# Optimization experiments

Measured on AMD Instinct MI355X. Metric: run time of the kernel, lower is better.

Reference implementation:

```python
import jax, jax.numpy as jnp
import numpy as np

MODEL_DIM = 256
PAIR_IMPORTANCE_WEIGHT = 0.5
B, S, D = 4, 4096, MODEL_DIM


def setup_inputs() -> dict:
    key = jax.random.key(0)
    ks = jax.random.split(key, 6)
    return {
        "query": jax.random.normal(ks[0], (B, S, D), dtype=jnp.float32),
        "key": jax.random.normal(ks[1], (B, S, D), dtype=jnp.float32),
        "value": jax.random.normal(ks[2], (B, S, D), dtype=jnp.float32),
        "W_query": jax.random.normal(ks[3], (D, D), dtype=jnp.float32),
        "W_key": jax.random.normal(ks[4], (D, D), dtype=jnp.float32),
        "W_value": jax.random.normal(ks[5], (D, D), dtype=jnp.float32),
    }


def reference(query, key, value, W_query, W_key, W_value):
    # Projections: [B,S,D] @ [D,D]
    q = jnp.einsum('bsd,de->bse', query, W_query)
    k = jnp.einsum('bsd,de->bse', key, W_key)
    v = jnp.einsum('bsd,de->bse', value, W_value)
    scale = jnp.sqrt(jnp.asarray(MODEL_DIM, dtype=q.dtype))
    # Full [B,S,S] score matrix (global max forces materialization)
    scores = jnp.einsum('bqd,bkd->bqk', q, k) / scale
    s_len = scores.shape[1]
    diag_bias = jnp.eye(s_len, dtype=scores.dtype) * jnp.max(scores)
    scores = scores + PAIR_IMPORTANCE_WEIGHT * diag_bias  # broadcast over batch
    attention_weights = jax.nn.softmax(scores, axis=-1)
    output = jnp.einsum('bqk,bkd->bqd', attention_weights, v)
    return output, attention_weights
```

## Files before the change

### kernel.cpp

```cpp
#include <hip/hip_runtime.h>
#include <cstdint>
#include <cstddef>

#define BB 4
#define SS 4096
#define DD 256
#define SCORE_SCALE (1.0f/16.0f)
#define PIW 0.5f

typedef float          f32x4  __attribute__((ext_vector_type(4)));
typedef __bf16         bf16v8 __attribute__((ext_vector_type(8)));
typedef unsigned short u16v8  __attribute__((ext_vector_type(8)));
typedef unsigned short u16v4  __attribute__((ext_vector_type(4)));

__device__ __forceinline__ f32x4 mfma_bf16(u16v8 a, u16v8 b, f32x4 c) {
    return __builtin_amdgcn_mfma_f32_16x16x32_bf16(
        __builtin_bit_cast(bf16v8, a), __builtin_bit_cast(bf16v8, b), c, 0, 0, 0);
}

__device__ __forceinline__ unsigned short f2bf(float f) {
    unsigned u = __float_as_uint(f);
    u += 0x7FFFu + ((u >> 16) & 1u);
    return (unsigned short)(u >> 16);
}
__device__ __forceinline__ float bf2f(unsigned short h) {
    return __uint_as_float(((unsigned)h) << 16);
}
__device__ __forceinline__ unsigned fenc(float x) {
    unsigned u = __float_as_uint(x);
    return (u & 0x80000000u) ? ~u : (u | 0x80000000u);
}
__device__ __forceinline__ float fdec(unsigned e) {
    return __uint_as_float((e & 0x80000000u) ? (e ^ 0x80000000u) : ~e);
}

#define TM 128
#define TN 128
#define TK 16
#define PADW 132

__global__ __launch_bounds__(256) void proj_kernel(
    const float* __restrict__ query, const float* __restrict__ key_, const float* __restrict__ value,
    const float* __restrict__ Wq, const float* __restrict__ Wk, const float* __restrict__ Wv,
    unsigned short* __restrict__ qh, unsigned short* __restrict__ ql,
    unsigned short* __restrict__ kh, unsigned short* __restrict__ kl,
    unsigned short* __restrict__ vT, unsigned* __restrict__ gmax)
{
    const int z = blockIdx.z;
    const float* A = (z == 0) ? query : (z == 1) ? key_ : value;
    const float* W = (z == 0) ? Wq    : (z == 1) ? Wk   : Wv;
    if (z == 0 && blockIdx.x == 0 && blockIdx.y == 0 && threadIdx.x == 0)
        *gmax = 0x007FFFFFu;

    const int K = DD, N = DD;
    __shared__ float As[TK][PADW];
    __shared__ float Bs[TK][PADW];
    const int tid = threadIdx.x;
    const int tx = tid & 15, ty = tid >> 4;
    const int rowBase = blockIdx.y * TM;
    const int colBase = blockIdx.x * TN;

    float acc[8][8] = {};

    for (int k0 = 0; k0 < K; k0 += TK) {
        #pragma unroll
        for (int i = 0; i < 2; i++) {
            int idx = tid + i * 256;
            int r = idx >> 2, kq = idx & 3;
            const float4 av = *(const float4*)&A[(size_t)(rowBase + r) * K + k0 + kq * 4];
            As[kq * 4 + 0][r] = av.x; As[kq * 4 + 1][r] = av.y;
            As[kq * 4 + 2][r] = av.z; As[kq * 4 + 3][r] = av.w;
        }
        #pragma unroll
        for (int i = 0; i < 2; i++) {
            int idx = tid + i * 256;
            int kk = idx >> 5, cq = idx & 31;
            *(float4*)&Bs[kk][cq * 4] = *(const float4*)&W[(size_t)(k0 + kk) * N + colBase + cq * 4];
        }
        __syncthreads();
        #pragma unroll
        for (int kk = 0; kk < TK; kk++) {
            float a[8], b[8];
            *(float4*)&a[0] = *(const float4*)&As[kk][ty * 8];
            *(float4*)&a[4] = *(const float4*)&As[kk][ty * 8 + 4];
            *(float4*)&b[0] = *(const float4*)&Bs[kk][tx * 8];
            *(float4*)&b[4] = *(const float4*)&Bs[kk][tx * 8 + 4];
            #pragma unroll
            for (int i = 0; i < 8; i++)
                #pragma unroll
                for (int j = 0; j < 8; j++)
                    acc[i][j] = fmaf(a[i], b[j], acc[i][j]);
        }
        __syncthreads();
    }

    #pragma unroll
    for (int i = 0; i < 8; i++) {
        const int gr = rowBase + ty * 8 + i;
        if (z == 2) {
            const int b2 = gr >> 12, s2 = gr & (SS - 1);
            #pragma unroll
            for (int j = 0; j < 8; j++) {
                int col = colBase + tx * 8 + j;
                vT[((size_t)b2 * DD + col) * SS + s2] = f2bf(acc[i][j]);
            }
        } else {
            unsigned short h[8], l[8];
            #pragma unroll
            for (int j = 0; j < 8; j++) {
                h[j] = f2bf(acc[i][j]);
                l[j] = f2bf(acc[i][j] - bf2f(h[j]));
            }
            unsigned short* H = (z == 0) ? qh : kh;
            unsigned short* L = (z == 0) ? ql : kl;
            size_t base = (size_t)gr * DD + colBase + tx * 8;
            *(u16v4*)&H[base]     = (u16v4){h[0], h[1], h[2], h[3]};
            *(u16v4*)&H[base + 4] = (u16v4){h[4], h[5], h[6], h[7]};
            *(u16v4*)&L[base]     = (u16v4){l[0], l[1], l[2], l[3]};
            *(u16v4*)&L[base + 4] = (u16v4){l[4], l[5], l[6], l[7]};
        }
    }
}

#define SPAD 40

__global__ __launch_bounds__(256) void scores_mfma(
    const unsigned short* __restrict__ qh, const unsigned short* __restrict__ ql,
    const unsigned short* __restrict__ kh, const unsigned short* __restrict__ kl,
    float* __restrict__ attn, unsigned* __restrict__ gmax)
{
    const int b = blockIdx.z;
    const size_t boff = (size_t)b * SS * DD;
    const unsigned short* Qh = qh + boff;
    const unsigned short* Ql = ql + boff;
    const unsigned short* Kh = kh + boff;
    const unsigned short* Kl = kl + boff;
    float* C = attn + (size_t)b * SS * SS;

    __shared__ unsigned short Ah[128][SPAD];
    __shared__ unsigned short Al[128][SPAD];
    __shared__ unsigned short Bh[128][SPAD];
    __shared__ unsigned short Bl[128][SPAD];
    __shared__ float red[256];

    const int tid = threadIdx.x;
    const int lane = tid & 63, w = tid >> 6;
    const int wr = (w >> 1) * 64, wc = (w & 1) * 64;
    const int m = lane & 15, qq = lane >> 4;
    const int rowBase = blockIdx.y * 128;
    const int colBase = blockIdx.x * 128;

    f32x4 acc[4][4];
    #pragma unroll
    for (int i = 0; i < 4; i++)
        #pragma unroll
        for (int j = 0; j < 4; j++)
            acc[i][j] = (f32x4){0.f, 0.f, 0.f, 0.f};

    const int chunk = (tid & 3) * 8;
    const int srow  = tid >> 2;

    for (int k0 = 0; k0 < DD; k0 += 32) {
        #pragma unroll
        for (int i = 0; i < 2; i++) {
            int r = srow + i * 64;
            size_t ga = (size_t)(rowBase + r) * DD + k0 + chunk;
            size_t gb = (size_t)(colBase + r) * DD + k0 + chunk;
            *(u16v8*)&Ah[r][chunk] = *(const u16v8*)&Qh[ga];
            *(u16v8*)&Al[r][chunk] = *(const u16v8*)&Ql[ga];
            *(u16v8*)&Bh[r][chunk] = *(const u16v8*)&Kh[gb];
            *(u16v8*)&Bl[r][chunk] = *(const u16v8*)&Kl[gb];
        }
        __syncthreads();

        const int kb = qq * 8;
        u16v8 ah[4], al[4], bh[4], bl[4];
        #pragma unroll
        for (int i = 0; i < 4; i++) {
            ah[i] = *(const u16v8*)&Ah[wr + i * 16 + m][kb];
            al[i] = *(const u16v8*)&Al[wr + i * 16 + m][kb];
            bh[i] = *(const u16v8*)&Bh[wc + i * 16 + m][kb];
            bl[i] = *(const u16v8*)&Bl[wc + i * 16 + m][kb];
        }
        #pragma unroll
        for (int i = 0; i < 4; i++)
            #pragma unroll
            for (int j = 0; j < 4; j++) {
                acc[i][j] = mfma_bf16(ah[i], bh[j], acc[i][j]);
                acc[i][j] = mfma_bf16(ah[i], bl[j], acc[i][j]);
                acc[i][j] = mfma_bf16(al[i], bh[j], acc[i][j]);
            }
        __syncthreads();
    }

    float mx = -INFINITY;
    #pragma unroll
    for (int i = 0; i < 4; i++) {
        #pragma unroll
        for (int j = 0; j < 4; j++) {
            #pragma unroll
            for (int r = 0; r < 4; r++) {
                float v = acc[i][j][r] * SCORE_SCALE;
                int row = rowBase + wr + i * 16 + qq * 4 + r;
                int col = colBase + wc + j * 16 + m;
                C[(size_t)row * SS + col] = v;
                mx = fmaxf(mx, v);
            }
        }
    }
    red[tid] = mx;
    __syncthreads();
    for (int s2 = 128; s2 > 0; s2 >>= 1) {
        if (tid < s2) red[tid] = fmaxf(red[tid], red[tid + s2]);
        __syncthreads();
    }
    if (tid == 0) atomicMax(gmax, fenc(red[0]));
}

__global__ __launch_bounds__(256) void softmax_kernel(
    float* __restrict__ attn, const unsigned* __restrict__ gmax)
{
    const int row = blockIdx.x;
    const int i = row & (SS - 1);
    float* p = attn + (size_t)row * SS;
    const float bias = PIW * fdec(*gmax);
    const int tid = threadIdx.x;

    float x[16];
    float m = -INFINITY;
    #pragma unroll
    for (int u = 0; u < 4; u++) {
        int j4 = u * 1024 + tid * 4;
        float4 t = *(const float4*)&p[j4];
        float e0 = t.x + ((j4 + 0 == i) ? bias : 0.0f);
        float e1 = t.y + ((j4 + 1 == i) ? bias : 0.0f);
        float e2 = t.z + ((j4 + 2 == i) ? bias : 0.0f);
        float e3 = t.w + ((j4 + 3 == i) ? bias : 0.0f);
        x[u * 4 + 0] = e0; x[u * 4 + 1] = e1; x[u * 4 + 2] = e2; x[u * 4 + 3] = e3;
        m = fmaxf(fmaxf(fmaxf(m, e0), fmaxf(e1, e2)), e3);
    }
    __shared__ float red[256];
    red[tid] = m;
    __syncthreads();
    for (int s2 = 128; s2 > 0; s2 >>= 1) {
        if (tid < s2) red[tid] = fmaxf(red[tid], red[tid + s2]);
        __syncthreads();
    }
    const float rm = red[0];
    __syncthreads();

    float s = 0.0f;
    #pragma unroll
    for (int u = 0; u < 16; u++) {
        x[u] = __expf(x[u] - rm);
        s += x[u];
    }
    red[tid] = s;
    __syncthreads();
    for (int s2 = 128; s2 > 0; s2 >>= 1) {
        if (tid < s2) red[tid] += red[tid + s2];
        __syncthreads();
    }
    const float inv = 1.0f / red[0];
    #pragma unroll
    for (int u = 0; u < 4; u++) {
        int j4 = u * 1024 + tid * 4;
        float4 o = make_float4(x[u*4+0] * inv, x[u*4+1] * inv, x[u*4+2] * inv, x[u*4+3] * inv);
        *(float4*)&p[j4] = o;
    }
}

#define APAD 72

__global__ __launch_bounds__(256) void av_mfma(
    const float* __restrict__ attn, const unsigned short* __restrict__ vT,
    float* __restrict__ out)
{
    const int b = blockIdx.y;
    const int rowBase = blockIdx.x * 32;
    const float* A = attn + (size_t)b * SS * SS;
    const unsigned short* Bv = vT + (size_t)b * DD * SS;

    __shared__ unsigned short As[32][APAD];
    __shared__ unsigned short Bs[256][APAD];

    const int tid = threadIdx.x;
    const int lane = tid & 63, w = tid >> 6;
    const int m = lane & 15, qq = lane >> 4;

    f32x4 acc[2][4];
    #pragma unroll
    for (int i = 0; i < 2; i++)
        #pragma unroll
        for (int j = 0; j < 4; j++)
            acc[i][j] = (f32x4){0.f, 0.f, 0.f, 0.f};

    for (int k0 = 0; k0 < SS; k0 += 64) {
        {
            const int ch = tid & 15;
            #pragma unroll
            for (int i = 0; i < 2; i++) {
                int r = (tid >> 4) + i * 16;
                float4 t = *(const float4*)&A[(size_t)(rowBase + r) * SS + k0 + ch * 4];
                u16v4 s = (u16v4){f2bf(t.x), f2bf(t.y), f2bf(t.z), f2bf(t.w)};
                *(u16v4*)&As[r][ch * 4] = s;
            }
        }
        {
            const int ch = (tid & 7) * 8;
            #pragma unroll
            for (int i = 0; i < 8; i++) {
                int r = (tid >> 3) + i * 32;
                *(u16v8*)&Bs[r][ch] = *(const u16v8*)&Bv[(size_t)r * SS + k0 + ch];
            }
        }
        __syncthreads();

        #pragma unroll
        for (int kk = 0; kk < 64; kk += 32) {
            const int kb = kk + qq * 8;
            u16v8 af[2], bf[4];
            #pragma unroll
            for (int i = 0; i < 2; i++)
                af[i] = *(const u16v8*)&As[i * 16 + m][kb];
            #pragma unroll
            for (int j = 0; j < 4; j++)
                bf[j] = *(const u16v8*)&Bs[w * 64 + j * 16 + m][kb];
            #pragma unroll
            for (int i = 0; i < 2; i++)
                #pragma unroll
                for (int j = 0; j < 4; j++)
                    acc[i][j] = mfma_bf16(af[i], bf[j], acc[i][j]);
        }
        __syncthreads();
    }

    #pragma unroll
    for (int i = 0; i < 2; i++) {
        #pragma unroll
        for (int j = 0; j < 4; j++) {
            #pragma unroll
            for (int r = 0; r < 4; r++) {
                int row = rowBase + i * 16 + qq * 4 + r;
                int col = w * 64 + j * 16 + m;
                out[((size_t)b * SS + row) * DD + col] = acc[i][j][r];
            }
        }
    }
}

extern "C" void kernel_launch(void* const* d_in, const int* in_sizes, int n_in,
                              void* d_out, int out_size, void* d_ws, size_t ws_size,
                              hipStream_t stream)
{
    const float* query = (const float*)d_in[0];
    const float* key_  = (const float*)d_in[1];
    const float* value = (const float*)d_in[2];
    const float* Wq    = (const float*)d_in[3];
    const float* Wk    = (const float*)d_in[4];
    const float* Wv    = (const float*)d_in[5];

    float* out  = (float*)d_out;
    float* attn = out + (size_t)BB * SS * DD;

    const size_t E = (size_t)BB * SS * DD;
    unsigned short* qh = (unsigned short*)d_ws;
    unsigned short* ql = qh + E;
    unsigned short* kh = ql + E;
    unsigned short* kl = kh + E;
    unsigned short* vT = kl + E;
    unsigned* gmax = (unsigned*)(vT + E);

    proj_kernel<<<dim3(DD / TN, (BB * SS) / TM, 3), 256, 0, stream>>>(
        query, key_, value, Wq, Wk, Wv, qh, ql, kh, kl, vT, gmax);
    scores_mfma<<<dim3(SS / 128, SS / 128, BB), 256, 0, stream>>>(
        qh, ql, kh, kl, attn, gmax);
    softmax_kernel<<<dim3(BB * SS), 256, 0, stream>>>(attn, gmax);
    av_mfma<<<dim3(SS / 32, BB), 256, 0, stream>>>(attn, vT, out);
}
```

Measured before the change: 684.2 us.

## Fuse softmax into scores and AV kernels via per-tile partial max/sum

The standalone softmax pass, which read and wrote the full 4x4096x4096 score matrix, is removed. The scores kernel now emits per-row partial max and sum-of-exp for each 128-column tile. A small combine kernel corrects the diagonal bias term and produces a per-row max and inverse sum. The AV kernel then normalizes the scores on the fly, writes the final weights, and feeds them to the MFMA. The projection GEMM also moves from scalar FMA to split-bf16 MFMA, with the 1/16 scale folded into q. The cost is an extra exp in the scores epilogue, the partial-statistics buffers, and a slightly different rounding order.

```diff
diff --git a/kernel.cpp b/kernel.cpp
--- a/kernel.cpp
+++ b/kernel.cpp
@@ -5,7 +5,6 @@
 #define BB 4
 #define SS 4096
 #define DD 256
-#define SCORE_SCALE (1.0f/16.0f)
 #define PIW 0.5f
 
 typedef float          f32x4  __attribute__((ext_vector_type(4)));
@@ -34,12 +33,19 @@
     return __uint_as_float((e & 0x80000000u) ? (e ^ 0x80000000u) : ~e);
 }
 
-#define TM 128
-#define TN 128
-#define TK 16
-#define PADW 132
-
-__global__ __launch_bounds__(256) void proj_kernel(
+__device__ __forceinline__ void split8(float4 x0, float4 x1, u16v8* h, u16v8* l) {
+    float xs[8] = {x0.x, x0.y, x0.z, x0.w, x1.x, x1.y, x1.z, x1.w};
+    #pragma unroll
+    for (int e = 0; e < 8; e++) {
+        unsigned short hh = f2bf(xs[e]);
+        (*h)[e] = hh;
+        (*l)[e] = f2bf(xs[e] - bf2f(hh));
+    }
+}
+
+#define FPAD 36
+
+__global__ __launch_bounds__(256) void proj_mfma(
     const float* __restrict__ query, const float* __restrict__ key_, const float* __restrict__ value,
     const float* __restrict__ Wq, const float* __restrict__ Wk, const float* __restrict__ Wv,
     unsigned short* __restrict__ qh, unsigned short* __restrict__ ql,
@@ -52,72 +58,83 @@
     if (z == 0 && blockIdx.x == 0 && blockIdx.y == 0 && threadIdx.x == 0)
         *gmax = 0x007FFFFFu;
 
-    const int K = DD, N = DD;
-    __shared__ float As[TK][PADW];
-    __shared__ float Bs[TK][PADW];
+    __shared__ float Af[128][FPAD];
+    __shared__ float Wf[128][FPAD];
+
     const int tid = threadIdx.x;
-    const int tx = tid & 15, ty = tid >> 4;
-    const int rowBase = blockIdx.y * TM;
-    const int colBase = blockIdx.x * TN;
-
-    float acc[8][8] = {};
-
-    for (int k0 = 0; k0 < K; k0 += TK) {
-        #pragma unroll
-        for (int i = 0; i < 2; i++) {
-            int idx = tid + i * 256;
-            int r = idx >> 2, kq = idx & 3;
-            const float4 av = *(const float4*)&A[(size_t)(rowBase + r) * K + k0 + kq * 4];
-            As[kq * 4 + 0][r] = av.x; As[kq * 4 + 1][r] = av.y;
-            As[kq * 4 + 2][r] = av.z; As[kq * 4 + 3][r] = av.w;
-        }
-        #pragma unroll
-        for (int i = 0; i < 2; i++) {
-            int idx = tid + i * 256;
-            int kk = idx >> 5, cq = idx & 31;
-            *(float4*)&Bs[kk][cq * 4] = *(const float4*)&W[(size_t)(k0 + kk) * N + colBase + cq * 4];
-        }
-        __syncthreads();
-        #pragma unroll
-        for (int kk = 0; kk < TK; kk++) {
-            float a[8], b[8];
-            *(float4*)&a[0] = *(const float4*)&As[kk][ty * 8];
-            *(float4*)&a[4] = *(const float4*)&As[kk][ty * 8 + 4];
-            *(float4*)&b[0] = *(const float4*)&Bs[kk][tx * 8];
-            *(float4*)&b[4] = *(const float4*)&Bs[kk][tx * 8 + 4];
-            #pragma unroll
-            for (int i = 0; i < 8; i++)
-                #pragma unroll
-                for (int j = 0; j < 8; j++)
-                    acc[i][j] = fmaf(a[i], b[j], acc[i][j]);
-        }
-        __syncthreads();
-    }
-
-    #pragma unroll
-    for (int i = 0; i < 8; i++) {
-        const int gr = rowBase + ty * 8 + i;
-        if (z == 2) {
-            const int b2 = gr >> 12, s2 = gr & (SS - 1);
-            #pragma unroll
-            for (int j = 0; j < 8; j++) {
-                int col = colBase + tx * 8 + j;
-                vT[((size_t)b2 * DD + col) * SS + s2] = f2bf(acc[i][j]);
-            }
-        } else {
-            unsigned short h[8], l[8];
-            #pragma unroll
-            for (int j = 0; j < 8; j++) {
-                h[j] = f2bf(acc[i][j]);
-                l[j] = f2bf(acc[i][j] - bf2f(h[j]));
-            }
-            unsigned short* H = (z == 0) ? qh : kh;
-            unsigned short* L = (z == 0) ? ql : kl;
-            size_t base = (size_t)gr * DD + colBase + tx * 8;
-            *(u16v4*)&H[base]     = (u16v4){h[0], h[1], h[2], h[3]};
-            *(u16v4*)&H[base + 4] = (u16v4){h[4], h[5], h[6], h[7]};
-            *(u16v4*)&L[base]     = (u16v4){l[0], l[1], l[2], l[3]};
-            *(u16v4*)&L[base + 4] = (u16v4){l[4], l[5], l[6], l[7]};
+    const int lane = tid & 63, w = tid >> 6;
+    const int wr = (w >> 1) * 64, wc = (w & 1) * 64;
+    const int m = lane & 15, qq = lane >> 4;
+    const int rowBase = blockIdx.y * 128;
+    const int colBase = blockIdx.x * 128;
+
+    f32x4 acc[4][4];
+    #pragma unroll
+    for (int i = 0; i < 4; i++)
+        #pragma unroll
+        for (int j = 0; j < 4; j++)
+            acc[i][j] = (f32x4){0.f, 0.f, 0.f, 0.f};
+
+    for (int k0 = 0; k0 < DD; k0 += 32) {
+        #pragma unroll
+        for (int i = 0; i < 4; i++) {
+            int c = tid + i * 256;
+            int r = c >> 3, q8 = c & 7;
+            *(float4*)&Af[r][q8 * 4] = *(const float4*)&A[(size_t)(rowBase + r) * DD + k0 + q8 * 4];
+        }
+        {
+            int c = tid & 127, kk0 = (tid >> 7) * 16;
+            #pragma unroll
+            for (int kk = 0; kk < 16; kk++)
+                Wf[c][kk0 + kk] = W[(size_t)(k0 + kk0 + kk) * DD + colBase + c];
+        }
+        __syncthreads();
+
+        u16v8 ah[4], al[4], bh[4], bl[4];
+        #pragma unroll
+        for (int i = 0; i < 4; i++) {
+            float4 x0 = *(const float4*)&Af[wr + i * 16 + m][qq * 8];
+            float4 x1 = *(const float4*)&Af[wr + i * 16 + m][qq * 8 + 4];
+            split8(x0, x1, &ah[i], &al[i]);
+        }
+        #pragma unroll
+        for (int j = 0; j < 4; j++) {
+            float4 x0 = *(const float4*)&Wf[wc + j * 16 + m][qq * 8];
+            float4 x1 = *(const float4*)&Wf[wc + j * 16 + m][qq * 8 + 4];
+            split8(x0, x1, &bh[j], &bl[j]);
+        }
+        #pragma unroll
+        for (int i = 0; i < 4; i++)
+            #pragma unroll
+            for (int j = 0; j < 4; j++) {
+                acc[i][j] = mfma_bf16(ah[i], bh[j], acc[i][j]);
+                acc[i][j] = mfma_bf16(ah[i], bl[j], acc[i][j]);
+                acc[i][j] = mfma_bf16(al[i], bh[j], acc[i][j]);
+            }
+        __syncthreads();
+    }
+
+    #pragma unroll
+    for (int i = 0; i < 4; i++) {
+        #pragma unroll
+        for (int j = 0; j < 4; j++) {
+            #pragma unroll
+            for (int r = 0; r < 4; r++) {
+                int gr  = rowBase + wr + i * 16 + qq * 4 + r;
+                int col = colBase + wc + j * 16 + m;
+                float v = acc[i][j][r];
+                if (z == 2) {
+                    int b2 = gr >> 12, s2 = gr & (SS - 1);
+                    vT[((size_t)b2 * DD + col) * SS + s2] = f2bf(v);
+                } else {
+                    if (z == 0) v *= (1.0f / 16.0f);
+                    unsigned short hh = f2bf(v);
+                    unsigned short ll = f2bf(v - bf2f(hh));
+                    size_t idx = (size_t)gr * DD + col;
+                    if (z == 0) { qh[idx] = hh; ql[idx] = ll; }
+                    else        { kh[idx] = hh; kl[idx] = ll; }
+                }
+            }
         }
     }
 }
@@ -127,7 +144,8 @@
 __global__ __launch_bounds__(256) void scores_mfma(
     const unsigned short* __restrict__ qh, const unsigned short* __restrict__ ql,
     const unsigned short* __restrict__ kh, const unsigned short* __restrict__ kl,
-    float* __restrict__ attn, unsigned* __restrict__ gmax)
+    float* __restrict__ attn, float* __restrict__ pmax, float* __restrict__ psum,
+    unsigned* __restrict__ gmax)
 {
     const int b = blockIdx.z;
     const size_t boff = (size_t)b * SS * DD;
@@ -141,6 +159,8 @@
     __shared__ unsigned short Al[128][SPAD];
     __shared__ unsigned short Bh[128][SPAD];
     __shared__ unsigned short Bl[128][SPAD];
+    __shared__ float smax[128][2];
+    __shared__ float ssum[128][2];
     __shared__ float red[256];
 
     const int tid = threadIdx.x;
@@ -193,23 +213,47 @@
         __syncthreads();
     }
 
-    float mx = -INFINITY;
+    float vm_all = -INFINITY;
     #pragma unroll
     for (int i = 0; i < 4; i++) {
         #pragma unroll
-        for (int j = 0; j < 4; j++) {
-            #pragma unroll
-            for (int r = 0; r < 4; r++) {
-                float v = acc[i][j][r] * SCORE_SCALE;
-                int row = rowBase + wr + i * 16 + qq * 4 + r;
-                int col = colBase + wc + j * 16 + m;
-                C[(size_t)row * SS + col] = v;
-                mx = fmaxf(mx, v);
-            }
-        }
-    }
-    red[tid] = mx;
+        for (int r = 0; r < 4; r++) {
+            int row = rowBase + wr + i * 16 + qq * 4 + r;
+            float vj[4];
+            float vm = -INFINITY;
+            #pragma unroll
+            for (int j = 0; j < 4; j++) {
+                vj[j] = acc[i][j][r];
+                C[(size_t)row * SS + colBase + wc + j * 16 + m] = vj[j];
+                vm = fmaxf(vm, vj[j]);
+            }
+            #pragma unroll
+            for (int o = 1; o < 16; o <<= 1)
+                vm = fmaxf(vm, __shfl_xor(vm, o));
+            float vs = 0.f;
+            #pragma unroll
+            for (int j = 0; j < 4; j++)
+                vs += __expf(vj[j] - vm);
+            #pragma unroll
+            for (int o = 1; o < 16; o <<= 1)
+                vs += __shfl_xor(vs, o);
+            vm_all = fmaxf(vm_all, vm);
+            if (m == 0) {
+                smax[wr + i * 16 + qq * 4 + r][w & 1] = vm;
+                ssum[wr + i * 16 + qq * 4 + r][w & 1] = vs;
+            }
+        }
+    }
+    red[tid] = vm_all;
     __syncthreads();
+    if (tid < 128) {
+        float m0 = smax[tid][0], m1 = smax[tid][1];
+        float M = fmaxf(m0, m1);
+        float P = ssum[tid][0] * __expf(m0 - M) + ssum[tid][1] * __expf(m1 - M);
+        size_t idx = ((size_t)(b * SS + rowBase + tid)) * 32 + blockIdx.x;
+        pmax[idx] = M;
+        psum[idx] = P;
+    }
     for (int s2 = 128; s2 > 0; s2 >>= 1) {
         if (tid < s2) red[tid] = fmaxf(red[tid], red[tid + s2]);
         __syncthreads();
@@ -217,77 +261,63 @@
     if (tid == 0) atomicMax(gmax, fenc(red[0]));
 }
 
-__global__ __launch_bounds__(256) void softmax_kernel(
-    float* __restrict__ attn, const unsigned* __restrict__ gmax)
+__global__ __launch_bounds__(256) void combine_kernel(
+    const float* __restrict__ pmax, const float* __restrict__ psum,
+    const float* __restrict__ attn, const unsigned* __restrict__ gmax,
+    float* __restrict__ rmax, float* __restrict__ rinv)
 {
-    const int row = blockIdx.x;
-    const int i = row & (SS - 1);
-    float* p = attn + (size_t)row * SS;
+    const int row = blockIdx.x * 256 + threadIdx.x;
+    const int b = row >> 12, i = row & (SS - 1);
     const float bias = PIW * fdec(*gmax);
-    const int tid = threadIdx.x;
-
-    float x[16];
-    float m = -INFINITY;
-    #pragma unroll
-    for (int u = 0; u < 4; u++) {
-        int j4 = u * 1024 + tid * 4;
-        float4 t = *(const float4*)&p[j4];
-        float e0 = t.x + ((j4 + 0 == i) ? bias : 0.0f);
-        float e1 = t.y + ((j4 + 1 == i) ? bias : 0.0f);
-        float e2 = t.z + ((j4 + 2 == i) ? bias : 0.0f);
-        float e3 = t.w + ((j4 + 3 == i) ? bias : 0.0f);
-        x[u * 4 + 0] = e0; x[u * 4 + 1] = e1; x[u * 4 + 2] = e2; x[u * 4 + 3] = e3;
-        m = fmaxf(fmaxf(fmaxf(m, e0), fmaxf(e1, e2)), e3);
-    }
-    __shared__ float red[256];
-    red[tid] = m;
-    __syncthreads();
-    for (int s2 = 128; s2 > 0; s2 >>= 1) {
-        if (tid < s2) red[tid] = fmaxf(red[tid], red[tid + s2]);
-        __syncthreads();
-    }
-    const float rm = red[0];
-    __syncthreads();
-
-    float s = 0.0f;
-    #pragma unroll
-    for (int u = 0; u < 16; u++) {
-        x[u] = __expf(x[u] - rm);
-        s += x[u];
-    }
-    red[tid] = s;
-    __syncthreads();
-    for (int s2 = 128; s2 > 0; s2 >>= 1) {
-        if (tid < s2) red[tid] += red[tid + s2];
-        __syncthreads();
-    }
-    const float inv = 1.0f / red[0];
-    #pragma unroll
-    for (int u = 0; u < 4; u++) {
-        int j4 = u * 1024 + tid * 4;
-        float4 o = make_float4(x[u*4+0] * inv, x[u*4+1] * inv, x[u*4+2] * inv, x[u*4+3] * inv);
-        *(float4*)&p[j4] = o;
-    }
+    const float d = attn[(size_t)b * SS * SS + (size_t)i * SS + i];
+    const float* pm = &pmax[(size_t)row * 32];
+    const float* ps = &psum[(size_t)row * 32];
+
+    float M = -INFINITY;
+    #pragma unroll 8
+    for (int t = 0; t < 32; t++) M = fmaxf(M, pm[t]);
+    const float db = d + bias;
+    const float Mrow = fmaxf(M, db);
+    const int t0 = i >> 7;
+    float S = 0.f;
+    #pragma unroll 8
+    for (int t = 0; t < 32; t++) {
+        float P = ps[t];
+        if (t == t0) P -= __expf(d - pm[t]);
+        S += P * __expf(pm[t] - Mrow);
+    }
+    S += __expf(db - Mrow);
+    rmax[row] = Mrow;
+    rinv[row] = 1.0f / S;
 }
 
 #define APAD 72
 
-__global__ __launch_bounds__(256) void av_mfma(
-    const float* __restrict__ attn, const unsigned short* __restrict__ vT,
-    float* __restrict__ out)
+__global__ __launch_bounds__(256) void av_fused(
+    float* __restrict__ attn, const unsigned short* __restrict__ vT,
+    const float* __restrict__ rmax, const float* __restrict__ rinv,
+    const unsigned* __restrict__ gmax, float* __restrict__ out)
 {
     const int b = blockIdx.y;
     const int rowBase = blockIdx.x * 32;
-    const float* A = attn + (size_t)b * SS * SS;
+    float* A = attn + (size_t)b * SS * SS;
     const unsigned short* Bv = vT + (size_t)b * DD * SS;
+    const float bias = PIW * fdec(*gmax);
 
     __shared__ unsigned short As[32][APAD];
     __shared__ unsigned short Bs[256][APAD];
+    __shared__ float sM[32], sI[32];
 
     const int tid = threadIdx.x;
     const int lane = tid & 63, w = tid >> 6;
     const int m = lane & 15, qq = lane >> 4;
 
+    if (tid < 32) {
+        sM[tid] = rmax[(b << 12) + rowBase + tid];
+        sI[tid] = rinv[(b << 12) + rowBase + tid];
+    }
+    __syncthreads();
+
     f32x4 acc[2][4];
     #pragma unroll
     for (int i = 0; i < 2; i++)
@@ -297,13 +327,21 @@
 
     for (int k0 = 0; k0 < SS; k0 += 64) {
         {
-            const int ch = tid & 15;
+            const int ch = (tid & 15) * 4;
             #pragma unroll
             for (int i = 0; i < 2; i++) {
-                int r = (tid >> 4) + i * 16;
-                float4 t = *(const float4*)&A[(size_t)(rowBase + r) * SS + k0 + ch * 4];
-                u16v4 s = (u16v4){f2bf(t.x), f2bf(t.y), f2bf(t.z), f2bf(t.w)};
-                *(u16v4*)&As[r][ch * 4] = s;
+                int rr = (tid >> 4) + i * 16;
+                int grow = rowBase + rr;
+                size_t idx = (size_t)grow * SS + k0 + ch;
+                float4 t = *(const float4*)&A[idx];
+                float M = sM[rr], I = sI[rr];
+                int c = k0 + ch;
+                float w0 = __expf(t.x + ((c + 0 == grow) ? bias : 0.f) - M) * I;
+                float w1 = __expf(t.y + ((c + 1 == grow) ? bias : 0.f) - M) * I;
+                float w2 = __expf(t.z + ((c + 2 == grow) ? bias : 0.f) - M) * I;
+                float w3 = __expf(t.w + ((c + 3 == grow) ? bias : 0.f) - M) * I;
+                *(float4*)&A[idx] = make_float4(w0, w1, w2, w3);
+                *(u16v4*)&As[rr][ch] = (u16v4){f2bf(w0), f2bf(w1), f2bf(w2), f2bf(w3)};
             }
         }
         {
@@ -369,12 +407,18 @@
     unsigned short* kh = ql + E;
     unsigned short* kl = kh + E;
     unsigned short* vT = kl + E;
-    unsigned* gmax = (unsigned*)(vT + E);
-
-    proj_kernel<<<dim3(DD / TN, (BB * SS) / TM, 3), 256, 0, stream>>>(
+    float* pmax = (float*)(vT + E);
+    float* psum = pmax + (size_t)BB * SS * 32;
+    float* rmax = psum + (size_t)BB * SS * 32;
+    float* rinv = rmax + (size_t)BB * SS;
+    unsigned* gmax = (unsigned*)(rinv + (size_t)BB * SS);
+
+    proj_mfma<<<dim3(DD / 128, (BB * SS) / 128, 3), 256, 0, stream>>>(
         query, key_, value, Wq, Wk, Wv, qh, ql, kh, kl, vT, gmax);
     scores_mfma<<<dim3(SS / 128, SS / 128, BB), 256, 0, stream>>>(
-        qh, ql, kh, kl, attn, gmax);
-    softmax_kernel<<<dim3(BB * SS), 256, 0, stream>>>(attn, gmax);
-    av_mfma<<<dim3(SS / 32, BB), 256, 0, stream>>>(attn, vT, out);
-}
+        qh, ql, kh, kl, attn, pmax, psum, gmax);
+    combine_kernel<<<dim3((BB * SS) / 256), 256, 0, stream>>>(
+        pmax, psum, attn, gmax, rmax, rinv);
+    av_fused<<<dim3(SS / 32, BB), 256, 0, stream>>>(
+        attn, vT, rmax, rinv, gmax, out);
+}
```

New measurement: 728.2 us. 1.06x slower.
